# Kernel tuning notes

Measured on AMD Instinct MI355X. Metric: run time of the kernel, lower is better.

The kernel has to match this reference:

```python
import jax, jax.numpy as jnp
import numpy as np

B, T, C, H = 8, 2048, 1024, 128  # batch, seq (== block_size), embed_size, head_size


def setup_inputs() -> dict:
    key = jax.random.key(0)
    k1, k2, k3, k4 = jax.random.split(key, 4)
    x = jax.random.normal(k1, (B, T, C), dtype=jnp.float32)
    s = 1.0 / np.sqrt(C).astype(np.float32)
    Wq = jax.random.normal(k2, (C, H), dtype=jnp.float32) * s
    Wk = jax.random.normal(k3, (C, H), dtype=jnp.float32) * s
    Wv = jax.random.normal(k4, (C, H), dtype=jnp.float32) * s
    return {"x": x, "Wq": Wq, "Wk": Wk, "Wv": Wv}


def reference(x, Wq, Wk, Wv):
    # x: (B, T, C); projections are bias-free Linears -> x @ W
    Bs, Ts, Cs = x.shape
    q = x @ Wq  # (B, T, H)
    k = x @ Wk  # (B, T, H)
    v = x @ Wv  # (B, T, H)
    # NOTE: original scales by embed_size C ** -0.5, not head_size.
    sims = jnp.einsum('bth,bsh->bts', q, k) * (float(Cs) ** -0.5)  # (B, T, T)
    causal = jnp.tril(jnp.ones((Ts, Ts), dtype=bool))
    sims = jnp.where(causal[None, :, :], sims, -jnp.inf)
    attentions = jax.nn.softmax(sims, axis=-1)  # (B, T, T)
    return attentions @ v  # (B, T, H)
```

## Files before the change

### kernel.cpp

```cpp
#include <hip/hip_runtime.h>


#define B_ 8
#define T_ 2048
#define C_ 1024
#define H_ 128

typedef __attribute__((ext_vector_type(4))) float  f32x4;
typedef __attribute__((ext_vector_type(8))) __bf16 bf16x8;
typedef __attribute__((ext_vector_type(4))) __bf16 bf16x4;
typedef __attribute__((ext_vector_type(4))) short  short4v;

#define QSCALE (0.03125f * 1.44269504088896340736f)

static __device__ __forceinline__ short f2bf(float f) {
  union { __bf16 b; short s; } u;
  u.b = (__bf16)f;
  return u.s;
}

static __device__ __forceinline__ unsigned packbf2(float lo, float hi) {
  union { __bf16 b; unsigned short s; } a, c;
  a.b = (__bf16)lo; c.b = (__bf16)hi;
  return (unsigned)a.s | ((unsigned)c.s << 16);
}

static __device__ __forceinline__ size_t qk_idx(int t, int h, int nk) {
  return ((size_t)((t >> 4) * nk + (h >> 5)) << 9) + (((h >> 3) & 3) << 7)
       + ((t & 15) << 3) + (h & 7);
}
static __device__ __forceinline__ size_t v_idx(int h, int t) {
  return ((size_t)((t >> 4) * 8 + (h >> 4)) << 8) + ((h & 15) << 4) + (t & 15);
}

static __device__ __forceinline__ f32x4 mfma16(unsigned a0, unsigned a1,
                                               unsigned b0, unsigned b1, f32x4 c) {
#if __has_builtin(__builtin_amdgcn_mfma_f32_16x16x16_bf16)
  union { unsigned u[2]; bf16x4 v; } ua, ub;
  ua.u[0] = a0; ua.u[1] = a1; ub.u[0] = b0; ub.u[1] = b1;
  return __builtin_amdgcn_mfma_f32_16x16x16_bf16(ua.v, ub.v, c, 0, 0, 0);
#elif __has_builtin(__builtin_amdgcn_mfma_f32_16x16x16bf16_1k)
  union { unsigned u[2]; short4v v; } ua, ub;
  ua.u[0] = a0; ua.u[1] = a1; ub.u[0] = b0; ub.u[1] = b1;
  return __builtin_amdgcn_mfma_f32_16x16x16bf16_1k(ua.v, ub.v, c, 0, 0, 0);
#else
  union { unsigned u[2]; short4v v; } ua, ub;
  ua.u[0] = a0; ua.u[1] = a1; ub.u[0] = b0; ub.u[1] = b1;
  f32x4 d = c;
  asm volatile("v_mfma_f32_16x16x16_bf16 %0, %1, %2, %0"
               : "+v"(d) : "v"(ua.v), "v"(ub.v));
  return d;
#endif
}

__global__ void prep_wt(const float* __restrict__ Wq, const float* __restrict__ Wk,
                        const float* __restrict__ Wv, short* __restrict__ Wtf) {
  __shared__ float L[64 * 129];
  const int mtx = blockIdx.x >> 4, kc = blockIdx.x & 15;
  const int k0 = kc * 64;
  const float* W = (mtx == 0) ? Wq : (mtx == 1 ? Wk : Wv);
  const float s = (mtx == 0) ? QSCALE : 1.0f;
  for (int i = threadIdx.x; i < 64 * 128; i += 256) {
    int kk = i >> 7, c = i & 127;
    L[kk * 129 + c] = W[(size_t)(k0 + kk) * H_ + c] * s;
  }
  __syncthreads();
  for (int i = threadIdx.x; i < 128 * 64; i += 256) {
    int n = i >> 6, kk = i & 63;
    Wtf[qk_idx(mtx * 128 + n, k0 + kk, 32)] = f2bf(L[kk * 129 + n]);
  }
}

__global__ __launch_bounds__(256) void proj(const float* __restrict__ x,
                                            const short* __restrict__ Wtf,
                                            short* __restrict__ Qf,
                                            short* __restrict__ Kf,
                                            short* __restrict__ Vf) {
  __shared__ __align__(16) short At[2][64 * 128];
  const int tid = threadIdx.x, lane = tid & 63, wv = tid >> 6;
  const int cg = lane & 15, rg = lane >> 4;
  const int lane8 = lane << 3;
  const int g = (blockIdx.x & 7) * 64 + (blockIdx.x >> 3);
  const int mb = g >> 1, bn = g & 1;
  const int m0 = mb * 64;
  const int nfrag0 = bn * 12 + wv * 3;
  const float* xblk = x + (size_t)m0 * C_;

  f32x4 acc[4][3];
#pragma unroll
  for (int i = 0; i < 4; ++i)
#pragma unroll
    for (int j = 0; j < 3; ++j) {
      f32x4 z = {0.f, 0.f, 0.f, 0.f};
      acc[i][j] = z;
    }

  f32x4 ldr[4][2];

#define PLOAD(kt)                                                              \
  { _Pragma("unroll") for (int it = 0; it < 4; ++it) {                         \
      int ls = it * 256 + tid; int r = ls >> 4, sc = ls & 15;                  \
      const float* p = xblk + (size_t)r * C_ + (kt) * 128 + sc * 8;            \
      ldr[it][0] = *(const f32x4*)p; ldr[it][1] = *(const f32x4*)(p + 4);      \
  } }

#define PWRITE(bf)                                                             \
  { _Pragma("unroll") for (int it = 0; it < 4; ++it) {                         \
      int ls = it * 256 + tid; int r = ls >> 4, sc = ls & 15;                  \
      bf16x8 tv;                                                               \
      tv[0] = (__bf16)ldr[it][0][0]; tv[1] = (__bf16)ldr[it][0][1];            \
      tv[2] = (__bf16)ldr[it][0][2]; tv[3] = (__bf16)ldr[it][0][3];            \
      tv[4] = (__bf16)ldr[it][1][0]; tv[5] = (__bf16)ldr[it][1][1];            \
      tv[6] = (__bf16)ldr[it][1][2]; tv[7] = (__bf16)ldr[it][1][3];            \
      *(bf16x8*)&At[bf][r * 128 + ((sc ^ (r & 7)) << 3)] = tv;                 \
  } }

  PLOAD(0);
  PWRITE(0);
  __syncthreads();

  for (int kt = 0; kt < 8; ++kt) {
    const int cur = kt & 1;
    if (kt < 7) PLOAD(kt + 1);

#pragma unroll
    for (int ks = 0; ks < 4; ++ks) {
      bf16x8 af[4];
#pragma unroll
      for (int fm = 0; fm < 4; ++fm) {
        int r = fm * 16 + cg;
        int slot = (ks * 4 + rg) ^ (r & 7);
        af[fm] = *(const bf16x8*)&At[cur][r * 128 + (slot << 3)];
      }
#pragma unroll
      for (int nf = 0; nf < 3; ++nf) {
        bf16x8 bfr = *(const bf16x8*)&Wtf[((size_t)((nfrag0 + nf) * 32 + kt * 4 + ks) << 9) + lane8];
#pragma unroll
        for (int fm = 0; fm < 4; ++fm)
          acc[fm][nf] = __builtin_amdgcn_mfma_f32_16x16x32_bf16(af[fm], bfr, acc[fm][nf], 0, 0, 0);
      }
    }
    if (kt < 7) PWRITE(cur ^ 1);
    __syncthreads();
  }
#undef PLOAD
#undef PWRITE

#pragma unroll
  for (int fm = 0; fm < 4; ++fm) {
#pragma unroll
    for (int nf = 0; nf < 3; ++nf) {
      int n = (nfrag0 + nf) * 16 + cg;
      int rowm = m0 + fm * 16 + rg * 4;
      size_t boff = (size_t)(rowm >> 11) << 18;
      f32x4 v = acc[fm][nf];
      if (n < 128) {
#pragma unroll
        for (int r = 0; r < 4; ++r)
          Qf[boff + qk_idx((rowm + r) & 2047, n, 4)] = f2bf(v[r]);
      } else if (n < 256) {
#pragma unroll
        for (int r = 0; r < 4; ++r)
          Kf[boff + qk_idx((rowm + r) & 2047, n - 128, 4)] = f2bf(v[r]);
      } else {
#pragma unroll
        for (int r = 0; r < 4; ++r)
          Vf[boff + v_idx(n - 256, (rowm + r) & 2047)] = f2bf(v[r]);
      }
    }
  }
}

#define OCW 132
__global__ __launch_bounds__(256) void attn(const short* __restrict__ Qf,
                                            const short* __restrict__ Kf,
                                            const short* __restrict__ Vf,
                                            float* __restrict__ out) {
  __shared__ __align__(16) float OC[4][32 * OCW];
  __shared__ float Mml[4][32], Lml[4][32];
  const int tid = threadIdx.x, lane = tid & 63, wv = tid >> 6;
  const int cg = lane & 15, rg = lane >> 4;
  const int lane8 = lane << 3;
  const int bid = blockIdx.x;
  const int b = bid & 7;
  const int qg = 63 - (bid >> 3);
  const int q0 = qg << 5;
  const int NT = (q0 + 95) >> 6;
  const int SPW = (NT + 3) >> 2;
  const int t0 = wv * SPW;
  const int t1 = (t0 + SPW < NT) ? (t0 + SPW) : NT;

  const short* Qp = Qf + ((size_t)b << 18);
  const short* Kp = Kf + ((size_t)b << 18);
  const short* Vp = Vf + ((size_t)b << 18);
  const float NEG_INF = -__builtin_inff();

  bf16x8 qf[2][4];
#pragma unroll
  for (int qc = 0; qc < 2; ++qc)
#pragma unroll
    for (int ks = 0; ks < 4; ++ks)
      qf[qc][ks] = *(const bf16x8*)&Qp[((size_t)(((q0 >> 4) + qc) * 4 + ks) << 9) + lane8];

  f32x4 o[8][2];
#pragma unroll
  for (int f = 0; f < 8; ++f)
#pragma unroll
    for (int qc = 0; qc < 2; ++qc) { f32x4 z = {0.f, 0.f, 0.f, 0.f}; o[f][qc] = z; }
  float m[2] = {NEG_INF, NEG_INF}, lsum[2] = {0.0f, 0.0f};

  bf16x8 kf[4][4];
#define LOADK(t_)                                                              \
  { const short* ktp = Kp + (size_t)(t_) * 8192;                               \
    _Pragma("unroll") for (int nf_ = 0; nf_ < 4; ++nf_)                        \
    _Pragma("unroll") for (int ks_ = 0; ks_ < 4; ++ks_)                        \
      kf[nf_][ks_] = *(const bf16x8*)&ktp[((nf_ * 4 + ks_) << 9) + lane8]; }

  if (t0 < t1) LOADK(t0);

  for (int t = t0; t < t1; ++t) {
    const int kv0 = t * 64;
    const short* vtile = Vp + (size_t)t * 8192;

    f32x4 s[4][2];
#pragma unroll
    for (int nf = 0; nf < 4; ++nf)
#pragma unroll
      for (int qc = 0; qc < 2; ++qc) { f32x4 z = {0.f, 0.f, 0.f, 0.f}; s[nf][qc] = z; }

    __builtin_amdgcn_s_setprio(1);
#pragma unroll
    for (int nf = 0; nf < 4; ++nf)
#pragma unroll
      for (int ks = 0; ks < 4; ++ks) {
        s[nf][0] = __builtin_amdgcn_mfma_f32_16x16x32_bf16(kf[nf][ks], qf[0][ks], s[nf][0], 0, 0, 0);
        s[nf][1] = __builtin_amdgcn_mfma_f32_16x16x32_bf16(kf[nf][ks], qf[1][ks], s[nf][1], 0, 0, 0);
      }
    __builtin_amdgcn_s_setprio(0);

    if (t + 1 < t1) LOADK(t + 1);

    unsigned v0a[8], v0b[8];
#pragma unroll
    for (int hf = 0; hf < 8; ++hf) {
      const unsigned* vp = (const unsigned*)&vtile[(hf << 8) + (cg << 4) + (rg << 2)];
      v0a[hf] = vp[0]; v0b[hf] = vp[1];
    }

    if (t == NT - 1) {
#pragma unroll
      for (int nf = 0; nf < 4; ++nf)
#pragma unroll
        for (int qc = 0; qc < 2; ++qc)
#pragma unroll
          for (int r = 0; r < 4; ++r)
            if (kv0 + nf * 16 + rg * 4 + r > q0 + qc * 16 + cg) s[nf][qc][r] = NEG_INF;
    }

    unsigned pk[4][2][2];
#pragma unroll
    for (int qc = 0; qc < 2; ++qc) {
      float pm = s[0][qc][0];
#pragma unroll
      for (int nf = 0; nf < 4; ++nf)
#pragma unroll
        for (int r = 0; r < 4; ++r) pm = fmaxf(pm, s[nf][qc][r]);
      pm = fmaxf(pm, __shfl_xor(pm, 16));
      pm = fmaxf(pm, __shfl_xor(pm, 32));
      float mn = fmaxf(m[qc], pm);
      float sf = exp2f(m[qc] - mn);
      m[qc] = mn;
      lsum[qc] *= sf;
#pragma unroll
      for (int nf = 0; nf < 4; ++nf) {
        float p0 = exp2f(s[nf][qc][0] - mn), p1 = exp2f(s[nf][qc][1] - mn);
        float p2 = exp2f(s[nf][qc][2] - mn), p3 = exp2f(s[nf][qc][3] - mn);
        lsum[qc] += (p0 + p1) + (p2 + p3);
        pk[nf][qc][0] = packbf2(p0, p1);
        pk[nf][qc][1] = packbf2(p2, p3);
      }
#pragma unroll
      for (int f = 0; f < 8; ++f)
#pragma unroll
        for (int r = 0; r < 4; ++r) o[f][qc][r] *= sf;
    }

    __builtin_amdgcn_s_setprio(1);
#pragma unroll
    for (int hf = 0; hf < 8; ++hf) {
      o[hf][0] = mfma16(v0a[hf], v0b[hf], pk[0][0][0], pk[0][0][1], o[hf][0]);
      o[hf][1] = mfma16(v0a[hf], v0b[hf], pk[0][1][0], pk[0][1][1], o[hf][1]);
    }
#pragma unroll
    for (int nf = 1; nf < 4; ++nf) {
      const unsigned b00 = pk[nf][0][0], b01 = pk[nf][0][1];
      const unsigned b10 = pk[nf][1][0], b11 = pk[nf][1][1];
#pragma unroll
      for (int hf = 0; hf < 8; ++hf) {
        const unsigned* vp = (const unsigned*)&vtile[((nf * 8 + hf) << 8) + (cg << 4) + (rg << 2)];
        unsigned v0 = vp[0], v1 = vp[1];
        o[hf][0] = mfma16(v0, v1, b00, b01, o[hf][0]);
        o[hf][1] = mfma16(v0, v1, b10, b11, o[hf][1]);
      }
    }
    __builtin_amdgcn_s_setprio(0);
  }
#undef LOADK

#pragma unroll
  for (int qc = 0; qc < 2; ++qc) {
    lsum[qc] += __shfl_xor(lsum[qc], 16);
    lsum[qc] += __shfl_xor(lsum[qc], 32);
  }
  if (lane < 16) {
#pragma unroll
    for (int qc = 0; qc < 2; ++qc) {
      Mml[wv][qc * 16 + lane] = m[qc];
      Lml[wv][qc * 16 + lane] = lsum[qc];
    }
  }
#pragma unroll
  for (int hf = 0; hf < 8; ++hf)
#pragma unroll
    for (int qc = 0; qc < 2; ++qc)
      *(f32x4*)&OC[wv][(qc * 16 + cg) * OCW + hf * 16 + rg * 4] = o[hf][qc];
  __syncthreads();

  for (int i = tid; i < 32 * 128; i += 256) {
    int row = i >> 7, col = i & 127;
    float m0v = Mml[0][row], m1v = Mml[1][row], m2v = Mml[2][row], m3v = Mml[3][row];
    float ms = fmaxf(fmaxf(m0v, m1v), fmaxf(m2v, m3v));
    float accv = 0.f, lacc = 0.f;
#pragma unroll
    for (int w = 0; w < 4; ++w) {
      float sc = exp2f(Mml[w][row] - ms);
      lacc += sc * Lml[w][row];
      accv += sc * OC[w][row * OCW + col];
    }
    out[(size_t)(b * T_ + q0 + row) * H_ + col] = accv / lacc;
  }
}

extern "C" void kernel_launch(void* const* d_in, const int* in_sizes, int n_in,
                              void* d_out, int out_size, void* d_ws, size_t ws_size,
                              hipStream_t stream) {
  const float* x  = (const float*)d_in[0];
  const float* Wq = (const float*)d_in[1];
  const float* Wk = (const float*)d_in[2];
  const float* Wv = (const float*)d_in[3];
  float* out = (float*)d_out;
  char* ws = (char*)d_ws;

  short* Wtf = (short*)(ws);
  short* Qf  = (short*)(ws + ((size_t)1 << 20));
  short* Kf  = (short*)(ws + ((size_t)5 << 20));
  short* Vf  = (short*)(ws + ((size_t)9 << 20));

  prep_wt<<<dim3(48), dim3(256), 0, stream>>>(Wq, Wk, Wv, Wtf);
  proj<<<dim3(512), dim3(256), 0, stream>>>(x, Wtf, Qf, Kf, Vf);
  attn<<<dim3(512), dim3(256), 0, stream>>>(Qf, Kf, Vf, out);
}
```

Before: 75.63 us.

## Pair heavy and light causal query tiles per block; rescale softmax lazily

The attention kernel now launches 256 blocks of 512 threads. Each block runs two 4-wave groups: one on a long causal query tile (63-p) and one on a short one (p). This balances per-block work across CUs and removes the tail of uneven blocks. The two groups' partial results are merged in turn through the shared OC buffer, which adds extra barriers. The online softmax also skips rescaling the accumulators and running sum unless the new row max exceeds the old one by more than 8 (log2 units), trading some exponent headroom in the bf16 probabilities for fewer multiplies.

```diff
diff --git a/kernel.cpp b/kernel.cpp
--- a/kernel.cpp
+++ b/kernel.cpp
@@ -172,22 +172,25 @@
 }
 
 #define OCW 132
-__global__ __launch_bounds__(256) void attn(const short* __restrict__ Qf,
+__global__ __launch_bounds__(512) void attn(const short* __restrict__ Qf,
                                             const short* __restrict__ Kf,
                                             const short* __restrict__ Vf,
                                             float* __restrict__ out) {
   __shared__ __align__(16) float OC[4][32 * OCW];
-  __shared__ float Mml[4][32], Lml[4][32];
+  __shared__ float Mml[8][32], Lml[8][32];
   const int tid = threadIdx.x, lane = tid & 63, wv = tid >> 6;
   const int cg = lane & 15, rg = lane >> 4;
   const int lane8 = lane << 3;
   const int bid = blockIdx.x;
   const int b = bid & 7;
-  const int qg = 63 - (bid >> 3);
+  const int p = bid >> 3;
+  const int grp = wv >> 2;
+  const int wvl = wv & 3;
+  const int qg = grp ? p : (63 - p);
   const int q0 = qg << 5;
   const int NT = (q0 + 95) >> 6;
   const int SPW = (NT + 3) >> 2;
-  const int t0 = wv * SPW;
+  const int t0 = wvl * SPW;
   const int t1 = (t0 + SPW < NT) ? (t0 + SPW) : NT;
 
   const short* Qp = Qf + ((size_t)b << 18);
@@ -267,22 +270,25 @@
         for (int r = 0; r < 4; ++r) pm = fmaxf(pm, s[nf][qc][r]);
       pm = fmaxf(pm, __shfl_xor(pm, 16));
       pm = fmaxf(pm, __shfl_xor(pm, 32));
-      float mn = fmaxf(m[qc], pm);
-      float sf = exp2f(m[qc] - mn);
-      m[qc] = mn;
-      lsum[qc] *= sf;
+      if (!__all(pm <= m[qc] + 8.0f)) {
+        float mn = fmaxf(m[qc], pm);
+        float sf = exp2f(m[qc] - mn);
+        m[qc] = mn;
+        lsum[qc] *= sf;
+#pragma unroll
+        for (int f = 0; f < 8; ++f)
+#pragma unroll
+          for (int r = 0; r < 4; ++r) o[f][qc][r] *= sf;
+      }
+      float mq = m[qc];
 #pragma unroll
       for (int nf = 0; nf < 4; ++nf) {
-        float p0 = exp2f(s[nf][qc][0] - mn), p1 = exp2f(s[nf][qc][1] - mn);
-        float p2 = exp2f(s[nf][qc][2] - mn), p3 = exp2f(s[nf][qc][3] - mn);
+        float p0 = exp2f(s[nf][qc][0] - mq), p1 = exp2f(s[nf][qc][1] - mq);
+        float p2 = exp2f(s[nf][qc][2] - mq), p3 = exp2f(s[nf][qc][3] - mq);
         lsum[qc] += (p0 + p1) + (p2 + p3);
         pk[nf][qc][0] = packbf2(p0, p1);
         pk[nf][qc][1] = packbf2(p2, p3);
       }
-#pragma unroll
-      for (int f = 0; f < 8; ++f)
-#pragma unroll
-        for (int r = 0; r < 4; ++r) o[f][qc][r] *= sf;
     }
 
     __builtin_amdgcn_s_setprio(1);
@@ -319,25 +325,52 @@
       Lml[wv][qc * 16 + lane] = lsum[qc];
     }
   }
-#pragma unroll
-  for (int hf = 0; hf < 8; ++hf)
-#pragma unroll
-    for (int qc = 0; qc < 2; ++qc)
-      *(f32x4*)&OC[wv][(qc * 16 + cg) * OCW + hf * 16 + rg * 4] = o[hf][qc];
-  __syncthreads();
-
-  for (int i = tid; i < 32 * 128; i += 256) {
-    int row = i >> 7, col = i & 127;
-    float m0v = Mml[0][row], m1v = Mml[1][row], m2v = Mml[2][row], m3v = Mml[3][row];
-    float ms = fmaxf(fmaxf(m0v, m1v), fmaxf(m2v, m3v));
-    float accv = 0.f, lacc = 0.f;
-#pragma unroll
-    for (int w = 0; w < 4; ++w) {
-      float sc = exp2f(Mml[w][row] - ms);
-      lacc += sc * Lml[w][row];
-      accv += sc * OC[w][row * OCW + col];
-    }
-    out[(size_t)(b * T_ + q0 + row) * H_ + col] = accv / lacc;
+  if (grp == 0) {
+#pragma unroll
+    for (int hf = 0; hf < 8; ++hf)
+#pragma unroll
+      for (int qc = 0; qc < 2; ++qc)
+        *(f32x4*)&OC[wv][(qc * 16 + cg) * OCW + hf * 16 + rg * 4] = o[hf][qc];
+  }
+  __syncthreads();
+  {
+    const int qb = (63 - p) << 5;
+    for (int i = tid; i < 32 * 128; i += 512) {
+      int row = i >> 7, col = i & 127;
+      float ms = fmaxf(fmaxf(Mml[0][row], Mml[1][row]), fmaxf(Mml[2][row], Mml[3][row]));
+      float accv = 0.f, lacc = 0.f;
+#pragma unroll
+      for (int w = 0; w < 4; ++w) {
+        float sc = exp2f(Mml[w][row] - ms);
+        lacc += sc * Lml[w][row];
+        accv += sc * OC[w][row * OCW + col];
+      }
+      out[(size_t)(b * T_ + qb + row) * H_ + col] = accv / lacc;
+    }
+  }
+  __syncthreads();
+  if (grp == 1) {
+#pragma unroll
+    for (int hf = 0; hf < 8; ++hf)
+#pragma unroll
+      for (int qc = 0; qc < 2; ++qc)
+        *(f32x4*)&OC[wvl][(qc * 16 + cg) * OCW + hf * 16 + rg * 4] = o[hf][qc];
+  }
+  __syncthreads();
+  {
+    const int qb = p << 5;
+    for (int i = tid; i < 32 * 128; i += 512) {
+      int row = i >> 7, col = i & 127;
+      float ms = fmaxf(fmaxf(Mml[4][row], Mml[5][row]), fmaxf(Mml[6][row], Mml[7][row]));
+      float accv = 0.f, lacc = 0.f;
+#pragma unroll
+      for (int w = 0; w < 4; ++w) {
+        float sc = exp2f(Mml[4 + w][row] - ms);
+        lacc += sc * Lml[4 + w][row];
+        accv += sc * OC[w][row * OCW + col];
+      }
+      out[(size_t)(b * T_ + qb + row) * H_ + col] = accv / lacc;
+    }
   }
 }
 
@@ -358,5 +391,5 @@
 
   prep_wt<<<dim3(48), dim3(256), 0, stream>>>(Wq, Wk, Wv, Wtf);
   proj<<<dim3(512), dim3(256), 0, stream>>>(x, Wtf, Qf, Kf, Vf);
-  attn<<<dim3(512), dim3(256), 0, stream>>>(Qf, Kf, Vf, out);
-}
+  attn<<<dim3(256), dim3(512), 0, stream>>>(Qf, Kf, Vf, out);
+}
```

Result: faster. 69.30 us (-8.4%).
